# Kernel optimization log

Hardware: AMD Instinct MI355X
Metric: run time of the kernel (lower is better)

## Reference

```python
import jax, jax.numpy as jnp
import numpy as np

N_NODES = 100000
N_EDGES = 1600000
IN_C, HID_C, OUT_C = 128, 128, 128


def setup_inputs() -> dict:
    key = jax.random.key(0)
    k_x, k_e, k_w1, k_w2 = jax.random.split(key, 4)
    x = jax.random.normal(k_x, (N_NODES, IN_C), dtype=jnp.float32)
    edge_index = jax.random.randint(k_e, (2, N_EDGES), 0, N_NODES, dtype=jnp.int64)
    # Glorot-style init for GCNConv linear weights
    s1 = (6.0 / (IN_C + HID_C)) ** 0.5
    s2 = (6.0 / (HID_C + OUT_C)) ** 0.5
    W1 = jax.random.uniform(k_w1, (IN_C, HID_C), jnp.float32, -s1, s1)
    b1 = jnp.zeros((HID_C,), jnp.float32)
    W2 = jax.random.uniform(k_w2, (HID_C, OUT_C), jnp.float32, -s2, s2)
    b2 = jnp.zeros((OUT_C,), jnp.float32)
    return {"x": x, "edge_index": edge_index, "W1": W1, "b1": b1, "W2": W2, "b2": b2}


def gcn_conv(x, src, dst, W, b, num_nodes):
    # PyG GCNConv: linear transform, then sym-normalized aggregation with self-loops.
    h = x @ W                                   # [N, out]
    ones = jnp.ones_like(dst, dtype=h.dtype)
    # degree counts include the self-loop (+1)
    deg = jax.ops.segment_sum(ones, dst, num_segments=num_nodes) + 1.0
    inv_sqrt = jax.lax.rsqrt(deg)               # deg > 0 since self-loops
    coef = inv_sqrt[src] * inv_sqrt[dst]        # [E]
    msgs = h[src] * coef[:, None]               # [E, out] gather + scale
    agg = jax.ops.segment_sum(msgs, dst, num_segments=num_nodes)
    # self-loop contribution: coef = 1/deg for the (i,i) edge
    agg = agg + h * (inv_sqrt * inv_sqrt)[:, None]
    return agg + b


def reference(x, edge_index, W1, b1, W2, b2):
    src, dst = edge_index[0], edge_index[1]
    h = gcn_conv(x, src, dst, W1, b1, N_NODES)
    h = jax.nn.relu(h)
    out = gcn_conv(h, src, dst, W2, b2, N_NODES)
    return out
```

## Files before the change

kernel.cpp:

```cpp
#include <hip/hip_runtime.h>
#include <hip/hip_bf16.h>
#include <hip/hip_fp16.h>

#define N_NODES 100000
#define N_EDGES 1600000
#define C 128
#define NB 782
#define NC 256
#define EPC (N_EDGES / NC)

typedef _Float16 half8 __attribute__((ext_vector_type(8)));
typedef _Float16 half4v __attribute__((ext_vector_type(4)));
typedef float f32x4 __attribute__((ext_vector_type(4)));

__global__ __launch_bounds__(256) void init_count(const float* __restrict__ W1,
                                                  const float* __restrict__ W2,
                                                  _Float16* __restrict__ W1s,
                                                  _Float16* __restrict__ W2s,
                                                  const int* __restrict__ dst,
                                                  int* __restrict__ cnt) {
    __shared__ int hist[NB];
    if (blockIdx.x < 16) {
        int i = blockIdx.x * 256 + threadIdx.x;
        int which = i >> 11;
        int u = i & 2047;
        int lane = u & 63, l = lane & 15, q = lane >> 4;
        int ct = u >> 6, c = ct >> 3, t = ct & 7;
        const float* Wsrc = which ? W2 : W1;
        _Float16* Dst = which ? W2s : W1s;
        half8 v;
#pragma unroll
        for (int j = 0; j < 8; j++)
            v[j] = (_Float16)Wsrc[(c * 32 + q * 8 + j) * C + t * 16 + l];
        *(half8*)(Dst + (size_t)u * 8) = v;
    } else {
        int c = blockIdx.x - 16;
        int tid = threadIdx.x;
        for (int b = tid; b < NB; b += 256) hist[b] = 0;
        __syncthreads();
        int base = c * EPC;
        for (int i = tid; i < EPC; i += 256)
            atomicAdd(&hist[dst[base + i] >> 7], 1);
        __syncthreads();
        for (int b = tid; b < NB; b += 256) cnt[b * NC + c] = hist[b];
    }
}

__global__ __launch_bounds__(256) void scan_block2(int* __restrict__ a,
                                                   int* __restrict__ partial, int n) {
    __shared__ int s[256];
    int tid = threadIdx.x;
    int i = blockIdx.x * 256 + tid;
    int v = (i < n) ? a[i] : 0;
    s[tid] = v;
    __syncthreads();
    for (int off = 1; off < 256; off <<= 1) {
        int t = (tid >= off) ? s[tid - off] : 0;
        __syncthreads();
        s[tid] += t;
        __syncthreads();
    }
    if (i < n) a[i] = s[tid] - v;
    if (tid == 255) partial[blockIdx.x] = s[255];
}

__global__ __launch_bounds__(1024) void scan_partial_1024(int* __restrict__ partial, int n) {
    __shared__ int s[1024];
    int tid = threadIdx.x;
    int v = (tid < n) ? partial[tid] : 0;
    s[tid] = v;
    __syncthreads();
    for (int off = 1; off < 1024; off <<= 1) {
        int t = (tid >= off) ? s[tid - off] : 0;
        __syncthreads();
        s[tid] += t;
        __syncthreads();
    }
    if (tid < n) partial[tid] = s[tid] - v;
}

__global__ __launch_bounds__(256) void scan_add(int* __restrict__ a,
                                                const int* __restrict__ partial, int n) {
    int i = blockIdx.x * 256 + threadIdx.x;
    if (i < n) a[i] += partial[blockIdx.x];
}

__device__ __forceinline__ void gemm_compute_store(const _Float16* __restrict__ Wsw,
                                                   _Float16* __restrict__ out, int n,
                                                   int m0, int tid, _Float16* smem) {
    int lane = tid & 63;
    int w = tid >> 6;
    int l = lane & 15, q = lane >> 4;
    f32x4 acc[8] = {};

#pragma unroll
    for (int c = 0; c < 4; c++) {
        half8 af = *(const half8*)(smem + (w * 16 + l) * 128 + (((c * 4 + q) ^ l) * 8));
#pragma unroll
        for (int t = 0; t < 8; t++) {
            half8 bf = *(const half8*)(Wsw + (size_t)((c * 8 + t) * 64 + lane) * 8);
            acc[t] = __builtin_amdgcn_mfma_f32_16x16x32_f16(af, bf, acc[t], 0, 0, 0);
        }
    }

    __syncthreads();
    _Float16* cbuf = smem + w * 2176;
#pragma unroll
    for (int t = 0; t < 8; t++)
#pragma unroll
        for (int i = 0; i < 4; i++)
            cbuf[(q * 4 + i) * 136 + t * 16 + l] = (_Float16)acc[t][i];
    __syncthreads();
#pragma unroll
    for (int i = 0; i < 4; i++) {
        int r16 = i * 4 + q;
        int row = m0 + w * 16 + r16;
        if (row < n)
            *(half8*)(out + (size_t)row * C + l * 8) =
                *(const half8*)(cbuf + r16 * 136 + l * 8);
    }
}

__global__ __launch_bounds__(256) void fused_gemm_scatter(const float* __restrict__ x,
                                                          const _Float16* __restrict__ W1s,
                                                          _Float16* __restrict__ h16, int n,
                                                          const int* __restrict__ src,
                                                          const int* __restrict__ dst,
                                                          const int* __restrict__ S,
                                                          unsigned int* __restrict__ bpacked,
                                                          int nbG) {
    __shared__ _Float16 smem[8704];
    if ((int)blockIdx.x < nbG) {
        int tid = threadIdx.x;
        int m0 = blockIdx.x * 64;
        const float4* A4 = (const float4*)x;
#pragma unroll
        for (int p = 0; p < 8; p++) {
            int idx = p * 256 + tid;
            int r = idx >> 5, f4 = idx & 31;
            int row = m0 + r; if (row >= n) row = n - 1;
            float4 v = A4[(size_t)row * 32 + f4];
            int kg = f4 >> 1, hi = f4 & 1;
            half4v hv = {(_Float16)v.x, (_Float16)v.y, (_Float16)v.z, (_Float16)v.w};
            *(half4v*)(smem + r * 128 + ((kg ^ (r & 15)) * 8) + hi * 4) = hv;
        }
        __syncthreads();
        gemm_compute_store(W1s, h16, n, m0, tid, smem);
    } else {
        int c = blockIdx.x - nbG;
        int tid = threadIdx.x;
        int* off = (int*)smem;
        for (int b = tid; b < NB; b += 256) off[b] = S[b * NC + c];
        __syncthreads();
        int base = c * EPC;
        for (int i = tid; i < EPC; i += 256) {
            int s = src[base + i];
            int d = dst[base + i];
            int p = atomicAdd(&off[d >> 7], 1);
            bpacked[p] = ((unsigned int)(d & 127) << 17) | (unsigned int)s;
        }
    }
}

__global__ __launch_bounds__(256) void node_sort(const unsigned int* __restrict__ bpacked,
                                                 const int* __restrict__ S,
                                                 int* __restrict__ srcs,
                                                 int* __restrict__ rowptr,
                                                 float* __restrict__ isq) {
    __shared__ int hist[128];
    __shared__ int sc[128];
    __shared__ int off2[128];
    int b = blockIdx.x, tid = threadIdx.x;
    int beg = S[b * NC];
    int end = (b == NB - 1) ? N_EDGES : S[(b + 1) * NC];
    if (tid < 128) hist[tid] = 0;
    __syncthreads();
    for (int i = beg + tid; i < end; i += 256)
        atomicAdd(&hist[bpacked[i] >> 17], 1);
    __syncthreads();
    if (tid < 128) sc[tid] = hist[tid];
    __syncthreads();
    for (int off = 1; off < 128; off <<= 1) {
        int t = 0;
        if (tid < 128 && tid >= off) t = sc[tid - off];
        __syncthreads();
        if (tid < 128) sc[tid] += t;
        __syncthreads();
    }
    if (tid < 128) {
        int node = b * 128 + tid;
        int deg = hist[tid];
        int start = beg + sc[tid] - deg;
        off2[tid] = start;
        if (node < N_NODES) {
            rowptr[node] = start;
            isq[node] = rsqrtf((float)deg + 1.0f);
        }
    }
    if (b == 0 && tid == 0) rowptr[N_NODES] = N_EDGES;
    __syncthreads();
    for (int i = beg + tid; i < end; i += 256) {
        unsigned int rec = bpacked[i];
        int li = (int)(rec >> 17);
        int p = atomicAdd(&off2[li], 1);
        srcs[p] = (int)(rec & 0x1FFFFu);
    }
}

__global__ __launch_bounds__(256) void fused_agg_gemm(const _Float16* __restrict__ h,
                                                      const int* __restrict__ rowptr,
                                                      const int* __restrict__ srcs,
                                                      const float* __restrict__ isq,
                                                      const float* __restrict__ bias,
                                                      const _Float16* __restrict__ Wsw,
                                                      _Float16* __restrict__ out, int n) {
    __shared__ _Float16 smem[8704];
    int tid = threadIdx.x;
    int lane = tid & 63, w = tid >> 6;
    int q = lane >> 4, l16 = lane & 15;
    int cb = l16 * 8;
    int m0 = blockIdx.x * 64;

    float4 bv0 = *(const float4*)(bias + cb);
    float4 bv1 = *(const float4*)(bias + cb + 4);
    float bb[8] = {bv0.x, bv0.y, bv0.z, bv0.w, bv1.x, bv1.y, bv1.z, bv1.w};

#pragma unroll 1
    for (int t = 0; t < 16; t++) {
        int node = m0 + w * 16 + t;
        if (node >= n) node = n - 1;
        int beg = rowptr[node];
        int end = rowptr[node + 1];
        float iqd = isq[node];

        float acc[8] = {};
        int j = beg + q;
        for (; j + 12 < end; j += 16) {
            int s0 = srcs[j], s1 = srcs[j + 4], s2 = srcs[j + 8], s3 = srcs[j + 12];
            half8 h0 = *(const half8*)(h + (size_t)s0 * C + cb);
            half8 h1 = *(const half8*)(h + (size_t)s1 * C + cb);
            half8 h2 = *(const half8*)(h + (size_t)s2 * C + cb);
            half8 h3 = *(const half8*)(h + (size_t)s3 * C + cb);
            float c0 = isq[s0] * iqd;
            float c1 = isq[s1] * iqd;
            float c2 = isq[s2] * iqd;
            float c3 = isq[s3] * iqd;
#pragma unroll
            for (int k = 0; k < 8; k++) acc[k] += c0 * (float)h0[k];
#pragma unroll
            for (int k = 0; k < 8; k++) acc[k] += c1 * (float)h1[k];
#pragma unroll
            for (int k = 0; k < 8; k++) acc[k] += c2 * (float)h2[k];
#pragma unroll
            for (int k = 0; k < 8; k++) acc[k] += c3 * (float)h3[k];
        }
        for (; j < end; j += 4) {
            int s = srcs[j];
            half8 hv = *(const half8*)(h + (size_t)s * C + cb);
            float cf = isq[s] * iqd;
#pragma unroll
            for (int k = 0; k < 8; k++) acc[k] += cf * (float)hv[k];
        }

#pragma unroll
        for (int k = 0; k < 8; k++) {
            acc[k] += __shfl_xor(acc[k], 16, 64);
            acc[k] += __shfl_xor(acc[k], 32, 64);
        }

        if (q == 0) {
            float sc = iqd * iqd;
            half8 hd = *(const half8*)(h + (size_t)node * C + cb);
            half8 o;
#pragma unroll
            for (int k = 0; k < 8; k++) {
                float vv = acc[k] + sc * (float)hd[k] + bb[k];
                o[k] = (_Float16)fmaxf(vv, 0.f);
            }
            int r = w * 16 + t;
            *(half8*)(smem + r * 128 + ((l16 ^ t) * 8)) = o;
        }
    }
    gemm_compute_store(Wsw, out, n, m0, tid, smem);
}

template <bool RELU, typename OT>
__global__ __launch_bounds__(256) void aggregate(const _Float16* __restrict__ h,
                                                 const int* __restrict__ rowptr,
                                                 const int* __restrict__ srcs,
                                                 const float* __restrict__ isq,
                                                 const float* __restrict__ bias,
                                                 OT* __restrict__ out, int n) {
    int lane = threadIdx.x & 63;
    int wave = threadIdx.x >> 6;
    int node = blockIdx.x * 4 + wave;
    if (node >= n) return;

    int q   = lane >> 4;
    int l16 = lane & 15;
    int cb  = l16 * 8;

    int beg = rowptr[node];
    int end = rowptr[node + 1];
    float iqd = isq[node];

    float acc[8] = {};

    int j = beg + q;
    for (; j + 12 < end; j += 16) {
        int s0 = srcs[j], s1 = srcs[j + 4], s2 = srcs[j + 8], s3 = srcs[j + 12];
        half8 h0 = *(const half8*)(h + (size_t)s0 * C + cb);
        half8 h1 = *(const half8*)(h + (size_t)s1 * C + cb);
        half8 h2 = *(const half8*)(h + (size_t)s2 * C + cb);
        half8 h3 = *(const half8*)(h + (size_t)s3 * C + cb);
        float c0 = isq[s0] * iqd;
        float c1 = isq[s1] * iqd;
        float c2 = isq[s2] * iqd;
        float c3 = isq[s3] * iqd;
#pragma unroll
        for (int k = 0; k < 8; k++) acc[k] += c0 * (float)h0[k];
#pragma unroll
        for (int k = 0; k < 8; k++) acc[k] += c1 * (float)h1[k];
#pragma unroll
        for (int k = 0; k < 8; k++) acc[k] += c2 * (float)h2[k];
#pragma unroll
        for (int k = 0; k < 8; k++) acc[k] += c3 * (float)h3[k];
    }
    for (; j < end; j += 4) {
        int s = srcs[j];
        half8 hv = *(const half8*)(h + (size_t)s * C + cb);
        float cf = isq[s] * iqd;
#pragma unroll
        for (int k = 0; k < 8; k++) acc[k] += cf * (float)hv[k];
    }

#pragma unroll
    for (int k = 0; k < 8; k++) {
        acc[k] += __shfl_xor(acc[k], 16, 64);
        acc[k] += __shfl_xor(acc[k], 32, 64);
    }

    if (q == 0) {
        float sc = iqd * iqd;
        half8 hd = *(const half8*)(h + (size_t)node * C + cb);
        float4 bv0 = *(const float4*)(bias + cb);
        float4 bv1 = *(const float4*)(bias + cb + 4);
        float bb[8] = {bv0.x, bv0.y, bv0.z, bv0.w, bv1.x, bv1.y, bv1.z, bv1.w};
#pragma unroll
        for (int k = 0; k < 8; k++) {
            acc[k] += sc * (float)hd[k] + bb[k];
            if (RELU) acc[k] = fmaxf(acc[k], 0.f);
        }
        if constexpr (sizeof(OT) == 2) {
            half8 o;
#pragma unroll
            for (int k = 0; k < 8; k++) o[k] = (_Float16)acc[k];
            *(half8*)((_Float16*)out + (size_t)node * C + cb) = o;
        } else {
            float4 o0 = {acc[0], acc[1], acc[2], acc[3]};
            float4 o1 = {acc[4], acc[5], acc[6], acc[7]};
            *(float4*)((float*)out + (size_t)node * C + cb) = o0;
            *(float4*)((float*)out + (size_t)node * C + cb + 4) = o1;
        }
    }
}

extern "C" void kernel_launch(void* const* d_in, const int* in_sizes, int n_in,
                              void* d_out, int out_size, void* d_ws, size_t ws_size,
                              hipStream_t stream) {
    const float* x  = (const float*)d_in[0];
    const int* ei   = (const int*)d_in[1];
    const float* W1 = (const float*)d_in[2];
    const float* b1 = (const float*)d_in[3];
    const float* W2 = (const float*)d_in[4];
    const float* b2 = (const float*)d_in[5];
    float* out = (float*)d_out;

    const int N = N_NODES, E = N_EDGES;
    const int* src = ei;
    const int* dst = ei + E;

    char* ws = (char*)d_ws;
    size_t off = 0;
    auto alloc = [&](size_t bytes) {
        size_t o = off;
        off = (off + bytes + 255) & ~(size_t)255;
        return o;
    };
    _Float16* h16   = (_Float16*)(ws + alloc((size_t)N * C * 2));
    _Float16* hB16  = (_Float16*)(ws + alloc((size_t)N * C * 2));
    _Float16* W1s   = (_Float16*)(ws + alloc((size_t)C * C * 2));
    _Float16* W2s   = (_Float16*)(ws + alloc((size_t)C * C * 2));
    int*      cnt   = (int*)     (ws + alloc((size_t)NB * NC * 4));
    int*      part  = (int*)     (ws + alloc((size_t)1024 * 4));
    unsigned int* bpacked = (unsigned int*)(ws + alloc((size_t)E * 4));
    int*      srcs  = (int*)     (ws + alloc((size_t)E * 4));
    int*    rowptr  = (int*)     (ws + alloc((size_t)(N + 1) * 4));
    float*    isq   = (float*)   (ws + alloc((size_t)N * 4));
    (void)ws_size; (void)n_in; (void)in_sizes; (void)out_size;

    const int nbG = (N + 63) / 64;
    const int nS  = NB * NC;
    const int nbS = nS / 256;

    init_count<<<16 + NC, 256, 0, stream>>>(W1, W2, W1s, W2s, dst, cnt);

    scan_block2<<<nbS, 256, 0, stream>>>(cnt, part, nS);
    scan_partial_1024<<<1, 1024, 0, stream>>>(part, nbS);
    scan_add<<<nbS, 256, 0, stream>>>(cnt, part, nS);

    fused_gemm_scatter<<<nbG + NC, 256, 0, stream>>>(x, W1s, h16, N, src, dst, cnt,
                                                     bpacked, nbG);

    node_sort<<<NB, 256, 0, stream>>>(bpacked, cnt, srcs, rowptr, isq);

    fused_agg_gemm<<<nbG, 256, 0, stream>>>(h16, rowptr, srcs, isq, b1, W2s, hB16, N);

    aggregate<false, float><<<(N + 3) / 4, 256, 0, stream>>>(hB16, rowptr, srcs, isq, b2, out, N);
}
```

Baseline: 346.8 us.

## Unfuse layer-2 aggregation from GEMM, map one node per quarter-wave, drop scan_add

Removes the scan_add kernel by folding the block partial offsets into the scatter and node_sort reads. Splits the fused aggregate+GEMM kernel into a standalone aggregate (with ReLU) followed by a separate MFMA GEMM kernel, adding an extra fp16 intermediate buffer. Changes the aggregation mapping so each 16-lane group handles its own node instead of a wave splitting one node's edges across four quarters, which removes the cross-lane shuffle reductions and the q==0 masked epilogue. This raises node-level parallelism and occupancy, at the cost of extra global traffic for the intermediate and one more launch. Row boundaries of quarter-wave groups may diverge because node degrees differ.

```diff
diff --git a/kernel.cpp b/kernel.cpp
--- a/kernel.cpp
+++ b/kernel.cpp
@@ -79,12 +79,6 @@
     if (tid < n) partial[tid] = s[tid] - v;
 }
 
-__global__ __launch_bounds__(256) void scan_add(int* __restrict__ a,
-                                                const int* __restrict__ partial, int n) {
-    int i = blockIdx.x * 256 + threadIdx.x;
-    if (i < n) a[i] += partial[blockIdx.x];
-}
-
 __device__ __forceinline__ void gemm_compute_store(const _Float16* __restrict__ Wsw,
                                                    _Float16* __restrict__ out, int n,
                                                    int m0, int tid, _Float16* smem) {
@@ -127,6 +121,7 @@
                                                           const int* __restrict__ src,
                                                           const int* __restrict__ dst,
                                                           const int* __restrict__ S,
+                                                          const int* __restrict__ part,
                                                           unsigned int* __restrict__ bpacked,
                                                           int nbG) {
     __shared__ _Float16 smem[8704];
@@ -150,7 +145,7 @@
         int c = blockIdx.x - nbG;
         int tid = threadIdx.x;
         int* off = (int*)smem;
-        for (int b = tid; b < NB; b += 256) off[b] = S[b * NC + c];
+        for (int b = tid; b < NB; b += 256) off[b] = S[b * NC + c] + part[b];
         __syncthreads();
         int base = c * EPC;
         for (int i = tid; i < EPC; i += 256) {
@@ -163,7 +158,7 @@
 }
 
 __global__ __launch_bounds__(256) void node_sort(const unsigned int* __restrict__ bpacked,
-                                                 const int* __restrict__ S,
+                                                 const int* __restrict__ part,
                                                  int* __restrict__ srcs,
                                                  int* __restrict__ rowptr,
                                                  float* __restrict__ isq) {
@@ -171,8 +166,8 @@
     __shared__ int sc[128];
     __shared__ int off2[128];
     int b = blockIdx.x, tid = threadIdx.x;
-    int beg = S[b * NC];
-    int end = (b == NB - 1) ? N_EDGES : S[(b + 1) * NC];
+    int beg = part[b];
+    int end = (b == NB - 1) ? N_EDGES : part[b + 1];
     if (tid < 128) hist[tid] = 0;
     __syncthreads();
     for (int i = beg + tid; i < end; i += 256)
@@ -207,80 +202,21 @@
     }
 }
 
-__global__ __launch_bounds__(256) void fused_agg_gemm(const _Float16* __restrict__ h,
-                                                      const int* __restrict__ rowptr,
-                                                      const int* __restrict__ srcs,
-                                                      const float* __restrict__ isq,
-                                                      const float* __restrict__ bias,
-                                                      const _Float16* __restrict__ Wsw,
-                                                      _Float16* __restrict__ out, int n) {
+__global__ __launch_bounds__(256) void gemm_mfma(const _Float16* __restrict__ A,
+                                                 const _Float16* __restrict__ Wsw,
+                                                 _Float16* __restrict__ out, int n) {
     __shared__ _Float16 smem[8704];
     int tid = threadIdx.x;
-    int lane = tid & 63, w = tid >> 6;
-    int q = lane >> 4, l16 = lane & 15;
-    int cb = l16 * 8;
     int m0 = blockIdx.x * 64;
-
-    float4 bv0 = *(const float4*)(bias + cb);
-    float4 bv1 = *(const float4*)(bias + cb + 4);
-    float bb[8] = {bv0.x, bv0.y, bv0.z, bv0.w, bv1.x, bv1.y, bv1.z, bv1.w};
-
-#pragma unroll 1
-    for (int t = 0; t < 16; t++) {
-        int node = m0 + w * 16 + t;
-        if (node >= n) node = n - 1;
-        int beg = rowptr[node];
-        int end = rowptr[node + 1];
-        float iqd = isq[node];
-
-        float acc[8] = {};
-        int j = beg + q;
-        for (; j + 12 < end; j += 16) {
-            int s0 = srcs[j], s1 = srcs[j + 4], s2 = srcs[j + 8], s3 = srcs[j + 12];
-            half8 h0 = *(const half8*)(h + (size_t)s0 * C + cb);
-            half8 h1 = *(const half8*)(h + (size_t)s1 * C + cb);
-            half8 h2 = *(const half8*)(h + (size_t)s2 * C + cb);
-            half8 h3 = *(const half8*)(h + (size_t)s3 * C + cb);
-            float c0 = isq[s0] * iqd;
-            float c1 = isq[s1] * iqd;
-            float c2 = isq[s2] * iqd;
-            float c3 = isq[s3] * iqd;
-#pragma unroll
-            for (int k = 0; k < 8; k++) acc[k] += c0 * (float)h0[k];
-#pragma unroll
-            for (int k = 0; k < 8; k++) acc[k] += c1 * (float)h1[k];
-#pragma unroll
-            for (int k = 0; k < 8; k++) acc[k] += c2 * (float)h2[k];
-#pragma unroll
-            for (int k = 0; k < 8; k++) acc[k] += c3 * (float)h3[k];
-        }
-        for (; j < end; j += 4) {
-            int s = srcs[j];
-            half8 hv = *(const half8*)(h + (size_t)s * C + cb);
-            float cf = isq[s] * iqd;
-#pragma unroll
-            for (int k = 0; k < 8; k++) acc[k] += cf * (float)hv[k];
-        }
-
-#pragma unroll
-        for (int k = 0; k < 8; k++) {
-            acc[k] += __shfl_xor(acc[k], 16, 64);
-            acc[k] += __shfl_xor(acc[k], 32, 64);
-        }
-
-        if (q == 0) {
-            float sc = iqd * iqd;
-            half8 hd = *(const half8*)(h + (size_t)node * C + cb);
-            half8 o;
-#pragma unroll
-            for (int k = 0; k < 8; k++) {
-                float vv = acc[k] + sc * (float)hd[k] + bb[k];
-                o[k] = (_Float16)fmaxf(vv, 0.f);
-            }
-            int r = w * 16 + t;
-            *(half8*)(smem + r * 128 + ((l16 ^ t) * 8)) = o;
-        }
-    }
+#pragma unroll
+    for (int p = 0; p < 4; p++) {
+        int idx = p * 256 + tid;
+        int r = idx >> 4, kg = idx & 15;
+        int row = m0 + r; if (row >= n) row = n - 1;
+        half8 v = *(const half8*)(A + (size_t)row * C + kg * 8);
+        *(half8*)(smem + r * 128 + ((kg ^ (r & 15)) * 8)) = v;
+    }
+    __syncthreads();
     gemm_compute_store(Wsw, out, n, m0, tid, smem);
 }
 
@@ -293,22 +229,19 @@
                                                  OT* __restrict__ out, int n) {
     int lane = threadIdx.x & 63;
     int wave = threadIdx.x >> 6;
-    int node = blockIdx.x * 4 + wave;
-    if (node >= n) return;
-
-    int q   = lane >> 4;
+    int q = lane >> 4;
     int l16 = lane & 15;
-    int cb  = l16 * 8;
+    int cb = l16 * 8;
+    int node = blockIdx.x * 16 + wave * 4 + q;
 
     int beg = rowptr[node];
     int end = rowptr[node + 1];
     float iqd = isq[node];
 
     float acc[8] = {};
-
-    int j = beg + q;
-    for (; j + 12 < end; j += 16) {
-        int s0 = srcs[j], s1 = srcs[j + 4], s2 = srcs[j + 8], s3 = srcs[j + 12];
+    int j = beg;
+    for (; j + 3 < end; j += 4) {
+        int s0 = srcs[j], s1 = srcs[j + 1], s2 = srcs[j + 2], s3 = srcs[j + 3];
         half8 h0 = *(const half8*)(h + (size_t)s0 * C + cb);
         half8 h1 = *(const half8*)(h + (size_t)s1 * C + cb);
         half8 h2 = *(const half8*)(h + (size_t)s2 * C + cb);
@@ -326,7 +259,7 @@
 #pragma unroll
         for (int k = 0; k < 8; k++) acc[k] += c3 * (float)h3[k];
     }
-    for (; j < end; j += 4) {
+    for (; j < end; ++j) {
         int s = srcs[j];
         half8 hv = *(const half8*)(h + (size_t)s * C + cb);
         float cf = isq[s] * iqd;
@@ -334,34 +267,26 @@
         for (int k = 0; k < 8; k++) acc[k] += cf * (float)hv[k];
     }
 
+    float sc = iqd * iqd;
+    half8 hd = *(const half8*)(h + (size_t)node * C + cb);
+    float4 bv0 = *(const float4*)(bias + cb);
+    float4 bv1 = *(const float4*)(bias + cb + 4);
+    float bb[8] = {bv0.x, bv0.y, bv0.z, bv0.w, bv1.x, bv1.y, bv1.z, bv1.w};
 #pragma unroll
     for (int k = 0; k < 8; k++) {
-        acc[k] += __shfl_xor(acc[k], 16, 64);
-        acc[k] += __shfl_xor(acc[k], 32, 64);
-    }
-
-    if (q == 0) {
-        float sc = iqd * iqd;
-        half8 hd = *(const half8*)(h + (size_t)node * C + cb);
-        float4 bv0 = *(const float4*)(bias + cb);
-        float4 bv1 = *(const float4*)(bias + cb + 4);
-        float bb[8] = {bv0.x, bv0.y, bv0.z, bv0.w, bv1.x, bv1.y, bv1.z, bv1.w};
-#pragma unroll
-        for (int k = 0; k < 8; k++) {
-            acc[k] += sc * (float)hd[k] + bb[k];
-            if (RELU) acc[k] = fmaxf(acc[k], 0.f);
-        }
-        if constexpr (sizeof(OT) == 2) {
-            half8 o;
-#pragma unroll
-            for (int k = 0; k < 8; k++) o[k] = (_Float16)acc[k];
-            *(half8*)((_Float16*)out + (size_t)node * C + cb) = o;
-        } else {
-            float4 o0 = {acc[0], acc[1], acc[2], acc[3]};
-            float4 o1 = {acc[4], acc[5], acc[6], acc[7]};
-            *(float4*)((float*)out + (size_t)node * C + cb) = o0;
-            *(float4*)((float*)out + (size_t)node * C + cb + 4) = o1;
-        }
+        acc[k] += sc * (float)hd[k] + bb[k];
+        if (RELU) acc[k] = fmaxf(acc[k], 0.f);
+    }
+    if constexpr (sizeof(OT) == 2) {
+        half8 o;
+#pragma unroll
+        for (int k = 0; k < 8; k++) o[k] = (_Float16)acc[k];
+        *(half8*)((_Float16*)out + (size_t)node * C + cb) = o;
+    } else {
+        float4 o0 = {acc[0], acc[1], acc[2], acc[3]};
+        float4 o1 = {acc[4], acc[5], acc[6], acc[7]};
+        *(float4*)((float*)out + (size_t)node * C + cb) = o0;
+        *(float4*)((float*)out + (size_t)node * C + cb + 4) = o1;
     }
 }
 
@@ -389,6 +314,7 @@
     };
     _Float16* h16   = (_Float16*)(ws + alloc((size_t)N * C * 2));
     _Float16* hB16  = (_Float16*)(ws + alloc((size_t)N * C * 2));
+    _Float16* hC16  = (_Float16*)(ws + alloc((size_t)N * C * 2));
     _Float16* W1s   = (_Float16*)(ws + alloc((size_t)C * C * 2));
     _Float16* W2s   = (_Float16*)(ws + alloc((size_t)C * C * 2));
     int*      cnt   = (int*)     (ws + alloc((size_t)NB * NC * 4));
@@ -402,19 +328,21 @@
     const int nbG = (N + 63) / 64;
     const int nS  = NB * NC;
     const int nbS = nS / 256;
+    const int nbA = N / 16;
 
     init_count<<<16 + NC, 256, 0, stream>>>(W1, W2, W1s, W2s, dst, cnt);
 
     scan_block2<<<nbS, 256, 0, stream>>>(cnt, part, nS);
     scan_partial_1024<<<1, 1024, 0, stream>>>(part, nbS);
-    scan_add<<<nbS, 256, 0, stream>>>(cnt, part, nS);
 
     fused_gemm_scatter<<<nbG + NC, 256, 0, stream>>>(x, W1s, h16, N, src, dst, cnt,
-                                                     bpacked, nbG);
-
-    node_sort<<<NB, 256, 0, stream>>>(bpacked, cnt, srcs, rowptr, isq);
-
-    fused_agg_gemm<<<nbG, 256, 0, stream>>>(h16, rowptr, srcs, isq, b1, W2s, hB16, N);
-
-    aggregate<false, float><<<(N + 3) / 4, 256, 0, stream>>>(hB16, rowptr, srcs, isq, b2, out, N);
-}
+                                                     part, bpacked, nbG);
+
+    node_sort<<<NB, 256, 0, stream>>>(bpacked, part, srcs, rowptr, isq);
+
+    aggregate<true, _Float16><<<nbA, 256, 0, stream>>>(h16, rowptr, srcs, isq, b1, hB16, N);
+
+    gemm_mfma<<<nbG, 256, 0, stream>>>(hB16, W2s, hC16, N);
+
+    aggregate<false, float><<<nbA, 256, 0, stream>>>(hC16, rowptr, srcs, isq, b2, out, N);
+}
```

Result: faster. 317.7 us (-8.4%).
